# Kernel optimization log

Hardware: AMD Instinct MI355X
Metric: run time of the kernel (lower is better)

Reference implementation:

```python
import jax, jax.numpy as jnp
import numpy as np


def setup_inputs() -> dict:
    key = jax.random.key(0)
    k1, k2, k3 = jax.random.split(key, 3)
    x = jax.random.normal(k1, (8192, 2048), dtype=jnp.float32)
    w = jax.random.normal(k2, (4096, 2048), dtype=jnp.float32) * 0.02  # [out, in]
    b = jax.random.normal(k3, (4096,), dtype=jnp.float32) * 0.01
    return {"x": x, "w": w, "b": b}


def reference(x, w, b):
    # Straight-through binarization: forward uses sign(w), gradient flows as identity.
    binary_w = w + jax.lax.stop_gradient(jnp.sign(w) - w)  # [out, in], values in {-1, 0, 1}
    # F.linear: x @ W^T + b
    return jnp.einsum("ni,oi->no", x, binary_w) + b
```

## Files before the change

kernel.cpp:

```cpp
#include <hip/hip_runtime.h>
#include <hip/hip_bf16.h>
#include <stdint.h>

typedef __bf16 bf16x8 __attribute__((ext_vector_type(8)));
typedef float  f32x4  __attribute__((ext_vector_type(4)));


__device__ __forceinline__ uint32_t rn2_bf16(uint32_t lo, uint32_t hi) {
  uint32_t rlo = (lo + 0x7FFFu + ((lo >> 16) & 1u)) >> 16;
  uint32_t rhi = (hi + 0x7FFFu + ((hi >> 16) & 1u)) >> 16;
  return (rhi << 16) | (rlo & 0xFFFFu);
}

__device__ __forceinline__ uint32_t sign2_bf16(uint32_t lo, uint32_t hi) {
  uint32_t slo = (lo & 0x7FFFFFFFu) ? (0x3F80u | ((lo >> 16) & 0x8000u)) : 0u;
  uint32_t shi = (hi & 0x7FFFFFFFu) ? (0x3F80u | ((hi >> 16) & 0x8000u)) : 0u;
  return (shi << 16) | slo;
}

__device__ __forceinline__ void gl16(const void* g, void* l) {
  __builtin_amdgcn_global_load_lds(
      (const __attribute__((address_space(1))) uint32_t*)g,
      (__attribute__((address_space(3))) uint32_t*)l,
      16, 0, 0);
}


__global__ void cvt_prep(const uint4* __restrict__ x, uint4* __restrict__ xo, int nx8,
                         const uint4* __restrict__ w, uint4* __restrict__ wo, int nw8) {
  int stride = gridDim.x * blockDim.x;
  int total = nx8 + nw8;
  for (int i = blockIdx.x * blockDim.x + threadIdx.x; i < total; i += stride) {
    if (i < nx8) {
      uint4 a = x[2 * i + 0];
      uint4 b = x[2 * i + 1];
      uint4 o;
      o.x = rn2_bf16(a.x, a.y);
      o.y = rn2_bf16(a.z, a.w);
      o.z = rn2_bf16(b.x, b.y);
      o.w = rn2_bf16(b.z, b.w);
      xo[i] = o;
    } else {
      int j = i - nx8;
      uint4 a = w[2 * j + 0];
      uint4 b = w[2 * j + 1];
      uint4 o;
      o.x = sign2_bf16(a.x, a.y);
      o.y = sign2_bf16(a.z, a.w);
      o.z = sign2_bf16(b.x, b.y);
      o.w = sign2_bf16(b.z, b.w);
      wo[j] = o;
    }
  }
}


#define BARX()  asm volatile("s_barrier" ::: "memory")
#define VM0()   asm volatile("s_waitcnt vmcnt(0)" ::: "memory")
#define VMN4()  asm volatile("s_waitcnt vmcnt(4)" ::: "memory")
#define SWZ(x)  ((x) ^ ((((x) >> 7) & 7) << 4))

__global__ __launch_bounds__(512, 2) void gemm256(
    const uint16_t* __restrict__ A,
    const uint16_t* __restrict__ B,
    const float* __restrict__ bias,
    float* __restrict__ C,
    int M, int N, int K) {
  __shared__ alignas(16) uint8_t L[131072];
  uint8_t* Lb = L;

  const int tid  = threadIdx.x;
  const int lane = tid & 63;
  const int w    = tid >> 6;
  const int wr   = w >> 2;
  const int wc   = w & 3;
  const int r16  = lane & 15;
  const int kg   = lane >> 4;

  const int nbx = N >> 8;
  const int nwg = nbx * (M >> 8);
  const int bid = blockIdx.x;
  const int swb = (bid & 7) * (nwg >> 3) + (bid >> 3);
  const size_t m0 = (size_t)(swb / nbx) << 8;
  const size_t n0 = (size_t)(swb % nbx) << 8;

  const int NT = K >> 6;
  const size_t rowB = (size_t)K * 2;

  const int o0 = (w << 10) + (lane << 4);
  const int o1 = o0 + 8192;
  const int s0 = SWZ(o0);
  const int s1 = SWZ(o1);
  const size_t g0 = (size_t)(s0 >> 7) * rowB + (s0 & 127);
  const size_t g1 = (size_t)(s1 >> 7) * rowB + (s1 & 127);
  const char* Ab = (const char*)A + m0 * rowB;
  const char* Bb = (const char*)B + n0 * rowB;
  const size_t hiO = (size_t)128 * rowB;
  const int wB = w << 10;

  const int laneA = (wr * 128 + r16) * 128 + kg * 16;
  const int laneB = (wc * 64 + r16) * 128 + kg * 16;

#define STG(LOFF, SRC) do { \
    gl16((SRC) + g0, Lb + (LOFF) + wB); \
    gl16((SRC) + g1, Lb + (LOFF) + 8192 + wB); } while (0)

#define FRA(d, mi, ks) (*reinterpret_cast<const bf16x8*>( \
    Lb + (d) * 65536 + SWZ(laneA + (mi) * 2048 + (ks) * 64)))
#define FRB(d, ni, ks) (*reinterpret_cast<const bf16x8*>( \
    Lb + (d) * 65536 + 32768 + SWZ(laneB + (ni) * 2048 + (ks) * 64)))

  f32x4 acc[8][4] = {};

#define QM(A4, B4, MB) do { \
    __builtin_amdgcn_s_setprio(1); \
    _Pragma("unroll") \
    for (int mi2 = 0; mi2 < 4; ++mi2) \
      _Pragma("unroll") \
      for (int ni = 0; ni < 4; ++ni) \
        acc[(MB) + mi2][ni] = __builtin_amdgcn_mfma_f32_16x16x32_bf16( \
            A4[mi2], B4[ni], acc[(MB) + mi2][ni], 0, 0, 0); \
    __builtin_amdgcn_s_setprio(0); } while (0)

#define RDA(DST, d, base, ks) do { \
    _Pragma("unroll") \
    for (int i = 0; i < 4; ++i) DST[i] = FRA(d, (base) + i, ks); } while (0)
#define RDB(DST, d, ks) do { \
    _Pragma("unroll") \
    for (int i = 0; i < 4; ++i) DST[i] = FRB(d, i, ks); } while (0)

  STG(0,      Ab);
  STG(16384,  Ab + hiO);
  STG(32768,  Bb);
  STG(49152,  Bb + hiO);
  STG(98304,  Bb + 128);
  STG(114688, Bb + hiO + 128);
  VMN4();
  BARX();

  bf16x8 aLo[4], aHi[4], bA[4], bB[4];
  RDA(aLo, 0, 0, 0);
  RDB(bA, 0, 0);

  const int T = K >> 7;
  for (int t = 0; t < T; ++t) {
    const size_t c1 = (size_t)(2 * t + 1) * 128;
    const int k2i = 2 * t + 2, k3i = 2 * t + 3;
    const size_t c2 = (size_t)(k2i < NT ? k2i : NT - 1) * 128;
    const size_t c3 = (size_t)(k3i < NT ? k3i : NT - 1) * 128;

    QM(aLo, bA, 0);
    RDA(aHi, 0, 4, 0);
    STG(65536, Ab + c1);
    STG(81920, Ab + hiO + c1);
    BARX();

    QM(aHi, bA, 4);
    RDA(aLo, 0, 0, 1);
    RDB(bB, 0, 1);
    BARX();

    QM(aLo, bB, 0);
    RDA(aHi, 0, 4, 1);
    VM0();
    BARX();

    QM(aHi, bB, 4);
    RDA(aLo, 1, 0, 0);
    RDB(bA, 1, 0);
    STG(32768, Bb + c2);
    STG(49152, Bb + hiO + c2);
    BARX();

    QM(aLo, bA, 0);
    RDA(aHi, 1, 4, 0);
    STG(0, Ab + c2);
    STG(16384, Ab + hiO + c2);
    BARX();

    QM(aHi, bA, 4);
    RDA(aLo, 1, 0, 1);
    RDB(bB, 1, 1);
    BARX();

    QM(aLo, bB, 0);
    RDA(aHi, 1, 4, 1);
    VM0();
    BARX();

    QM(aHi, bB, 4);
    RDA(aLo, 0, 0, 0);
    RDB(bA, 0, 0);
    STG(98304, Bb + c3);
    STG(114688, Bb + hiO + c3);
    BARX();
  }

#pragma unroll
  for (int ni = 0; ni < 4; ++ni) {
    const size_t col = n0 + wc * 64 + ni * 16 + r16;
    const float bv = bias[col];
#pragma unroll
    for (int mi = 0; mi < 8; ++mi) {
      const size_t row0 = m0 + wr * 128 + mi * 16 + kg * 4;
#pragma unroll
      for (int j = 0; j < 4; ++j)
        C[(row0 + j) * N + col] = acc[mi][ni][j] + bv;
    }
  }
}


__global__ __launch_bounds__(256) void gemm_bin(
    const uint16_t* __restrict__ A, const uint16_t* __restrict__ B,
    const float* __restrict__ bias, float* __restrict__ C,
    int M, int N, int K) {
  constexpr int BK = 32;
  __shared__ alignas(16) uint16_t lA[128 * BK];
  __shared__ alignas(16) uint16_t lB[128 * BK];
  const int tid = threadIdx.x;
  const int lane = tid & 63;
  const int wid = tid >> 6;
  const int wr = wid >> 1, wc = wid & 1;
  const int r16 = lane & 15, kg = lane >> 4;
  const int m0 = blockIdx.y * 128, n0 = blockIdx.x * 128;
  f32x4 acc[4][4] = {};
  for (int k0 = 0; k0 < K; k0 += BK) {
    __syncthreads();
#pragma unroll
    for (int p = 0; p < 2; ++p) {
      int idx = p * 256 + tid;
      int row = idx >> 2;
      int col = (idx & 3) * 8;
      gl16(A + (size_t)(m0 + row) * K + k0 + col, lA + p * 2048 + wid * 512);
      gl16(B + (size_t)(n0 + row) * K + k0 + col, lB + p * 2048 + wid * 512);
    }
    __syncthreads();
    bf16x8 af[4], bg[4];
#pragma unroll
    for (int i = 0; i < 4; ++i)
      af[i] = *reinterpret_cast<const bf16x8*>(lA + (wr * 64 + i * 16 + r16) * BK + kg * 8);
#pragma unroll
    for (int i = 0; i < 4; ++i)
      bg[i] = *reinterpret_cast<const bf16x8*>(lB + (wc * 64 + i * 16 + r16) * BK + kg * 8);
#pragma unroll
    for (int mi = 0; mi < 4; ++mi)
#pragma unroll
      for (int ni = 0; ni < 4; ++ni)
        acc[mi][ni] = __builtin_amdgcn_mfma_f32_16x16x32_bf16(af[mi], bg[ni], acc[mi][ni], 0, 0, 0);
  }
#pragma unroll
  for (int ni = 0; ni < 4; ++ni) {
    int col = n0 + wc * 64 + ni * 16 + r16;
    float bv = bias[col];
#pragma unroll
    for (int mi = 0; mi < 4; ++mi) {
      int row0 = m0 + wr * 64 + mi * 16 + kg * 4;
#pragma unroll
      for (int j = 0; j < 4; ++j)
        C[(size_t)(row0 + j) * N + col] = acc[mi][ni][j] + bv;
    }
  }
}

__global__ void gemm_naive(const float* __restrict__ x, const float* __restrict__ w,
                           const float* __restrict__ b, float* __restrict__ out,
                           int M, int N, int K) {
  int n = blockIdx.x * blockDim.x + threadIdx.x;
  int m = blockIdx.y;
  if (n >= N || m >= M) return;
  float acc = 0.f;
  for (int k = 0; k < K; ++k) {
    float wv = w[(size_t)n * K + k];
    float s = (wv > 0.f) ? 1.f : ((wv < 0.f) ? -1.f : 0.f);
    acc += x[(size_t)m * K + k] * s;
  }
  out[(size_t)m * N + n] = acc + b[n];
}

extern "C" void kernel_launch(void* const* d_in, const int* in_sizes, int n_in,
                              void* d_out, int out_size, void* d_ws, size_t ws_size,
                              hipStream_t stream) {
  const float* x = (const float*)d_in[0];
  const float* w = (const float*)d_in[1];
  const float* b = (const float*)d_in[2];
  float* out = (float*)d_out;

  const int N = in_sizes[2];
  const int K = in_sizes[1] / N;
  const int M = in_sizes[0] / K;

  const size_t need = ((size_t)M * K + (size_t)N * K) * sizeof(uint16_t);
  if (ws_size < need) {
    hipLaunchKernelGGL(gemm_naive, dim3((N + 255) / 256, M), dim3(256), 0, stream,
                       x, w, b, out, M, N, K);
    return;
  }

  uint16_t* Xb = (uint16_t*)d_ws;
  uint16_t* Wb = Xb + (size_t)M * K;

  hipLaunchKernelGGL(cvt_prep, dim3(2048), dim3(256), 0, stream,
                     (const uint4*)x, (uint4*)Xb, (M * K) / 8,
                     (const uint4*)w, (uint4*)Wb, (N * K) / 8);

  const bool big_ok = (M % 256 == 0) && (N % 256 == 0) && (K % 256 == 0) &&
                      (((M / 256) * (N / 256)) % 8 == 0);
  if (big_ok) {
    hipLaunchKernelGGL(gemm256, dim3((M / 256) * (N / 256)), dim3(512), 0, stream,
                       Xb, Wb, b, out, M, N, K);
  } else {
    hipLaunchKernelGGL(gemm_bin, dim3(N / 128, M / 128), dim3(256), 0, stream,
                       Xb, Wb, b, out, M, N, K);
  }
}
```

Before: 147.0 us.

## Switch GEMM to 32x32x16 MFMA with fragment-ordered LDS layout

Replaces the 16x16x32 bf16 MFMA tiling with 32x32x16 MFMA (4x2 tiles of 32x32 per wave). Global-to-LDS staging now writes each k-slice straight into the per-lane fragment order the MFMA wants, so reads are contiguous 16-byte lane loads and the XOR swizzle is gone. The larger MFMA halves the instruction count and needs fewer LDS fragment loads per flop. In exchange, the staged global reads are less contiguous per row, the LDS layout may bring new bank patterns, and the epilogue store pattern changes.

```diff
diff --git a/kernel.cpp b/kernel.cpp
--- a/kernel.cpp
+++ b/kernel.cpp
@@ -4,6 +4,7 @@
 
 typedef __bf16 bf16x8 __attribute__((ext_vector_type(8)));
 typedef float  f32x4  __attribute__((ext_vector_type(4)));
+typedef float  f32x16 __attribute__((ext_vector_type(16)));
 
 
 __device__ __forceinline__ uint32_t rn2_bf16(uint32_t lo, uint32_t hi) {
@@ -58,7 +59,6 @@
 #define BARX()  asm volatile("s_barrier" ::: "memory")
 #define VM0()   asm volatile("s_waitcnt vmcnt(0)" ::: "memory")
 #define VMN4()  asm volatile("s_waitcnt vmcnt(4)" ::: "memory")
-#define SWZ(x)  ((x) ^ ((((x) >> 7) & 7) << 4))
 
 __global__ __launch_bounds__(512, 2) void gemm256(
     const uint16_t* __restrict__ A,
@@ -74,8 +74,9 @@
   const int w    = tid >> 6;
   const int wr   = w >> 2;
   const int wc   = w & 3;
-  const int r16  = lane & 15;
-  const int kg   = lane >> 4;
+  const int l31  = lane & 31;
+  const int lhi  = lane >> 5;
+  const int lds16 = lane * 16;
 
   const int nbx = N >> 8;
   const int nwg = nbx * (M >> 8);
@@ -87,47 +88,40 @@
   const int NT = K >> 6;
   const size_t rowB = (size_t)K * 2;
 
-  const int o0 = (w << 10) + (lane << 4);
-  const int o1 = o0 + 8192;
-  const int s0 = SWZ(o0);
-  const int s1 = SWZ(o1);
-  const size_t g0 = (size_t)(s0 >> 7) * rowB + (s0 & 127);
-  const size_t g1 = (size_t)(s1 >> 7) * rowB + (s1 & 127);
+  const size_t vStg = (size_t)((w >> 1) * 32 + l31) * rowB + (w & 1) * 64 + lhi * 16;
+  const int dStg = w * 2048;
+
   const char* Ab = (const char*)A + m0 * rowB;
   const char* Bb = (const char*)B + n0 * rowB;
   const size_t hiO = (size_t)128 * rowB;
-  const int wB = w << 10;
-
-  const int laneA = (wr * 128 + r16) * 128 + kg * 16;
-  const int laneB = (wc * 64 + r16) * 128 + kg * 16;
 
 #define STG(LOFF, SRC) do { \
-    gl16((SRC) + g0, Lb + (LOFF) + wB); \
-    gl16((SRC) + g1, Lb + (LOFF) + 8192 + wB); } while (0)
-
-#define FRA(d, mi, ks) (*reinterpret_cast<const bf16x8*>( \
-    Lb + (d) * 65536 + SWZ(laneA + (mi) * 2048 + (ks) * 64)))
-#define FRB(d, ni, ks) (*reinterpret_cast<const bf16x8*>( \
-    Lb + (d) * 65536 + 32768 + SWZ(laneB + (ni) * 2048 + (ks) * 64)))
-
-  f32x4 acc[8][4] = {};
-
-#define QM(A4, B4, MB) do { \
+    gl16((SRC) + vStg, Lb + (LOFF) + dStg); \
+    gl16((SRC) + vStg + 32, Lb + (LOFF) + dStg + 1024); } while (0)
+
+#define FRA32(d, i, q) (*reinterpret_cast<const bf16x8*>( \
+    Lb + (d) * 65536 + wr * 16384 + (i) * 4096 + (q) * 1024 + lds16))
+#define FRB32(d, j, q) (*reinterpret_cast<const bf16x8*>( \
+    Lb + (d) * 65536 + 32768 + wc * 8192 + (j) * 4096 + (q) * 1024 + lds16))
+
+#define RDA(DST, d, q) do { \
+    _Pragma("unroll") \
+    for (int i = 0; i < 4; ++i) DST[i] = FRA32(d, i, q); } while (0)
+#define RDB(DST, d, q) do { \
+    _Pragma("unroll") \
+    for (int j = 0; j < 2; ++j) DST[j] = FRB32(d, j, q); } while (0)
+
+  f32x16 acc[4][2] = {};
+
+#define QM(A4, B2) do { \
     __builtin_amdgcn_s_setprio(1); \
     _Pragma("unroll") \
-    for (int mi2 = 0; mi2 < 4; ++mi2) \
+    for (int i = 0; i < 4; ++i) \
       _Pragma("unroll") \
-      for (int ni = 0; ni < 4; ++ni) \
-        acc[(MB) + mi2][ni] = __builtin_amdgcn_mfma_f32_16x16x32_bf16( \
-            A4[mi2], B4[ni], acc[(MB) + mi2][ni], 0, 0, 0); \
+      for (int j = 0; j < 2; ++j) \
+        acc[i][j] = __builtin_amdgcn_mfma_f32_32x32x16_bf16( \
+            A4[i], B2[j], acc[i][j], 0, 0, 0); \
     __builtin_amdgcn_s_setprio(0); } while (0)
-
-#define RDA(DST, d, base, ks) do { \
-    _Pragma("unroll") \
-    for (int i = 0; i < 4; ++i) DST[i] = FRA(d, (base) + i, ks); } while (0)
-#define RDB(DST, d, ks) do { \
-    _Pragma("unroll") \
-    for (int i = 0; i < 4; ++i) DST[i] = FRB(d, i, ks); } while (0)
 
   STG(0,      Ab);
   STG(16384,  Ab + hiO);
@@ -138,9 +132,9 @@
   VMN4();
   BARX();
 
-  bf16x8 aLo[4], aHi[4], bA[4], bB[4];
-  RDA(aLo, 0, 0, 0);
-  RDB(bA, 0, 0);
+  bf16x8 aP[4], aQ[4], bP[2], bQ[2];
+  RDA(aP, 0, 0);
+  RDB(bP, 0, 0);
 
   const int T = K >> 7;
   for (int t = 0; t < T; ++t) {
@@ -149,63 +143,61 @@
     const size_t c2 = (size_t)(k2i < NT ? k2i : NT - 1) * 128;
     const size_t c3 = (size_t)(k3i < NT ? k3i : NT - 1) * 128;
 
-    QM(aLo, bA, 0);
-    RDA(aHi, 0, 4, 0);
+    QM(aP, bP);
+    RDA(aQ, 0, 1); RDB(bQ, 0, 1);
     STG(65536, Ab + c1);
     STG(81920, Ab + hiO + c1);
     BARX();
 
-    QM(aHi, bA, 4);
-    RDA(aLo, 0, 0, 1);
-    RDB(bB, 0, 1);
-    BARX();
-
-    QM(aLo, bB, 0);
-    RDA(aHi, 0, 4, 1);
+    QM(aQ, bQ);
+    RDA(aP, 0, 2); RDB(bP, 0, 2);
+    BARX();
+
+    QM(aP, bP);
+    RDA(aQ, 0, 3); RDB(bQ, 0, 3);
     VM0();
     BARX();
 
-    QM(aHi, bB, 4);
-    RDA(aLo, 1, 0, 0);
-    RDB(bA, 1, 0);
+    QM(aQ, bQ);
+    RDA(aP, 1, 0); RDB(bP, 1, 0);
     STG(32768, Bb + c2);
     STG(49152, Bb + hiO + c2);
     BARX();
 
-    QM(aLo, bA, 0);
-    RDA(aHi, 1, 4, 0);
+    QM(aP, bP);
+    RDA(aQ, 1, 1); RDB(bQ, 1, 1);
     STG(0, Ab + c2);
     STG(16384, Ab + hiO + c2);
     BARX();
 
-    QM(aHi, bA, 4);
-    RDA(aLo, 1, 0, 1);
-    RDB(bB, 1, 1);
-    BARX();
-
-    QM(aLo, bB, 0);
-    RDA(aHi, 1, 4, 1);
+    QM(aQ, bQ);
+    RDA(aP, 1, 2); RDB(bP, 1, 2);
+    BARX();
+
+    QM(aP, bP);
+    RDA(aQ, 1, 3); RDB(bQ, 1, 3);
     VM0();
     BARX();
 
-    QM(aHi, bB, 4);
-    RDA(aLo, 0, 0, 0);
-    RDB(bA, 0, 0);
+    QM(aQ, bQ);
+    RDA(aP, 0, 0); RDB(bP, 0, 0);
     STG(98304, Bb + c3);
     STG(114688, Bb + hiO + c3);
     BARX();
   }
 
 #pragma unroll
-  for (int ni = 0; ni < 4; ++ni) {
-    const size_t col = n0 + wc * 64 + ni * 16 + r16;
-    const float bv = bias[col];
-#pragma unroll
-    for (int mi = 0; mi < 8; ++mi) {
-      const size_t row0 = m0 + wr * 128 + mi * 16 + kg * 4;
-#pragma unroll
-      for (int j = 0; j < 4; ++j)
-        C[(row0 + j) * N + col] = acc[mi][ni][j] + bv;
+  for (int i = 0; i < 4; ++i) {
+#pragma unroll
+    for (int j2 = 0; j2 < 2; ++j2) {
+      const size_t col = n0 + wc * 64 + j2 * 32 + l31;
+      const float bv = bias[col];
+      const size_t rbase = m0 + wr * 128 + i * 32 + lhi * 4;
+#pragma unroll
+      for (int r = 0; r < 16; ++r) {
+        const size_t row = rbase + (r & 3) + 8 * (r >> 2);
+        C[row * N + col] = acc[i][j2][r] + bv;
+      }
     }
   }
 }
```

Result: slower. 203.7 us (+38.6%).
